# Kernel tuning notes

Measured on AMD Instinct MI355X. Metric: run time of the kernel, lower is better.

## Reference

```python
import jax, jax.numpy as jnp
import numpy as np

H, DK, DV = 16, 64, 64

def setup_inputs() -> dict:
    key = jax.random.key(0)
    ks = jax.random.split(key, 5)
    S, E = 2048, 1024
    return {
        "x": jax.random.normal(ks[0], (S, E), jnp.float32),
        "Wq": jax.random.normal(ks[1], (H * DK, E), jnp.float32) * 0.02,
        "Wk": jax.random.normal(ks[2], (H * DK, E), jnp.float32) * 0.02,
        "Wv": jax.random.normal(ks[3], (H * DV, E), jnp.float32) * 0.02,
        "Wo": jax.random.normal(ks[4], (H * DV, H * DV), jnp.float32) * 0.02,
    }

def reference(x, Wq, Wk, Wv, Wo):
    S = x.shape[0]
    # Fused QKV projections (equivalent to per-head Linear with concatenated weights)
    Q = (x @ Wq.T).reshape(S, H, DK).transpose(1, 0, 2)  # [H,S,dk]
    K = (x @ Wk.T).reshape(S, H, DK).transpose(1, 0, 2)  # [H,S,dk]
    V = (x @ Wv.T).reshape(S, H, DV).transpose(1, 0, 2)  # [H,S,dv]
    scale = 1.0 / np.sqrt(DK).astype(np.float32)
    scores = jnp.einsum('hsd,htd->hst', Q, K) * scale    # [H,S,S]
    weights = jax.nn.softmax(scores, axis=-1)
    A = jnp.einsum('hst,htv->hsv', weights, V)           # [H,S,dv]
    A1 = A.transpose(1, 0, 2).reshape(S, H * DV)         # concat heads on last dim
    return A1 @ Wo.T
```

## Files before the change

### kernel.cpp

```cpp
#include <hip/hip_runtime.h>
#include <hip/hip_bf16.h>
#include <stdint.h>

typedef uint16_t u16;
typedef uint32_t u32;
typedef float    f32x4  __attribute__((ext_vector_type(4)));
typedef __bf16   bf16x8 __attribute__((ext_vector_type(8)));
typedef uint16_t u16x8  __attribute__((ext_vector_type(8)));
typedef uint16_t u16x4  __attribute__((ext_vector_type(4)));
typedef uint32_t u32x4  __attribute__((ext_vector_type(4)));

#define HH 16
#define SS 2048
#define EE 1024
#define DD 64

__device__ inline u16 f2bf(float f) {
  uint32_t u = __builtin_bit_cast(uint32_t, f);
  u += 0x7fff + ((u >> 16) & 1);
  return (u16)(u >> 16);
}
__device__ inline float bf2f(u16 b) {
  return __builtin_bit_cast(float, (uint32_t)b << 16);
}

__device__ inline u32 cvtpk(float lo, float hi) {
  u32 r;
  asm("v_cvt_pk_bf16_f32 %0, %1, %2" : "=v"(r) : "v"(lo), "v"(hi));
  return r;
}

__device__ inline void gload_lds16(const void* g, void* l) {
  __builtin_amdgcn_global_load_lds(
      (const __attribute__((address_space(1))) uint32_t*)g,
      (__attribute__((address_space(3))) uint32_t*)l, 16, 0, 0);
}

__global__ __launch_bounds__(256) void convert_kernel(
    const float* __restrict__ x,  const float* __restrict__ wq,
    const float* __restrict__ wk, const float* __restrict__ wv,
    const float* __restrict__ wo,
    u16* __restrict__ xb, u16* __restrict__ wqkvb, u16* __restrict__ wob) {
  const int64_t M1 = 1024 * 1024;
  int64_t e = ((int64_t)blockIdx.x * 256 + threadIdx.x) * 4;
  const float* src; u16* dst; int64_t off;
  if (e < 2 * M1)      { src = x;  dst = xb;           off = e; }
  else if (e < 3 * M1) { src = wq; dst = wqkvb;        off = e - 2 * M1; }
  else if (e < 4 * M1) { src = wk; dst = wqkvb + M1;   off = e - 3 * M1; }
  else if (e < 5 * M1) { src = wv; dst = wqkvb + 2*M1; off = e - 4 * M1; }
  else                 { src = wo; dst = wob;          off = e - 5 * M1; }
  float4 v = *(const float4*)(src + off);
  u16x4 o;
  o[0] = f2bf(v.x); o[1] = f2bf(v.y); o[2] = f2bf(v.z); o[3] = f2bf(v.w);
  *(u16x4*)(dst + off) = o;
}

template <int EPI>
__global__ __launch_bounds__(256, 4) void gemm_kernel(
    const u16* __restrict__ A, const u16* __restrict__ B, int K, int N,
    u16* __restrict__ q_ws, u16* __restrict__ k_ws, u16* __restrict__ vt_ws,
    float* __restrict__ Cout) {
  constexpr int BM = 64, BN = 128, BK = 64;
  __shared__ __align__(16) u16 As[BM * BK];
  __shared__ __align__(16) u16 Bs[BN * BK];
  const int t = threadIdx.x;
  const int lane = t & 63, w = t >> 6;
  const int wr = w >> 1, wc = w & 1;
  const int fr = lane & 15, fg = lane >> 4;

  const int nwg = gridDim.x * gridDim.y;
  const int bid = blockIdx.y * gridDim.x + blockIdx.x;
  const int swz = (bid & 7) * (nwg >> 3) + (bid >> 3);
  const int m0 = (swz / gridDim.x) * BM, n0 = (swz % gridDim.x) * BN;

  f32x4 acc[2][4] = {};

  for (int k0 = 0; k0 < K; k0 += BK) {
#pragma unroll
    for (int it = 0; it < 2; ++it) {
      const int c = t + it * 256, row = c >> 3, sch = (c & 7) ^ (row & 7);
      gload_lds16(A + (int64_t)(m0 + row) * K + k0 + sch * 8,
                  As + (c & ~63) * 8);
    }
#pragma unroll
    for (int it = 0; it < 4; ++it) {
      const int c = t + it * 256, row = c >> 3, sch = (c & 7) ^ (row & 7);
      gload_lds16(B + (int64_t)(n0 + row) * K + k0 + sch * 8,
                  Bs + (c & ~63) * 8);
    }
    __syncthreads();
    bf16x8 af[2][2], bfr[4][2];
#pragma unroll
    for (int mi = 0; mi < 2; ++mi)
#pragma unroll
      for (int kc = 0; kc < 2; ++kc) {
        const int row = wr * 32 + mi * 16 + fr;
        const int cc = (kc * 4 + fg) ^ (row & 7);
        af[mi][kc] = __builtin_bit_cast(bf16x8, *(const u16x8*)&As[row * 64 + cc * 8]);
      }
#pragma unroll
    for (int ni = 0; ni < 4; ++ni)
#pragma unroll
      for (int kc = 0; kc < 2; ++kc) {
        const int row = wc * 64 + ni * 16 + fr;
        const int cc = (kc * 4 + fg) ^ (row & 7);
        bfr[ni][kc] = __builtin_bit_cast(bf16x8, *(const u16x8*)&Bs[row * 64 + cc * 8]);
      }
#pragma unroll
    for (int kc = 0; kc < 2; ++kc)
#pragma unroll
      for (int mi = 0; mi < 2; ++mi)
#pragma unroll
        for (int ni = 0; ni < 4; ++ni)
          acc[mi][ni] = __builtin_amdgcn_mfma_f32_16x16x32_bf16(
              af[mi][kc], bfr[ni][kc], acc[mi][ni], 0, 0, 0);
    __syncthreads();
  }

#pragma unroll
  for (int mi = 0; mi < 2; ++mi)
#pragma unroll
    for (int ni = 0; ni < 4; ++ni)
#pragma unroll
      for (int r = 0; r < 4; ++r) {
        const int m = m0 + wr * 32 + mi * 16 + fg * 4 + r;
        const int n = n0 + wc * 64 + ni * 16 + fr;
        const float v = acc[mi][ni][r];
        if constexpr (EPI == 0) {
          const int which = n >> 10, nn = n & 1023, h = nn >> 6, d = nn & 63;
          const u16 bv = f2bf(v);
          if (which == 0)      q_ws[((int64_t)h * SS + m) * DD + d] = bv;
          else if (which == 1) k_ws[((int64_t)h * SS + m) * DD + d] = bv;
          else                 vt_ws[((int64_t)h * DD + d) * SS + m] = bv;
        } else {
          Cout[(int64_t)m * N + n] = v;
        }
      }
}

__global__ __launch_bounds__(256, 4) void attn_kernel(
    const u16* __restrict__ q_ws, const u16* __restrict__ k_ws,
    const u16* __restrict__ vt_ws, u16* __restrict__ opart,
    float2* __restrict__ ml) {
  constexpr int NT2 = SS / 64 / 2;
  __shared__ __align__(16) u16 Ks[2][64 * 64];
  __shared__ __align__(16) u16 Vs[2][64 * 64];
  const int t = threadIdx.x;
  const int lane = t & 63, w = t >> 6;
  const int ql = lane & 15, g = lane >> 4;
  const int h = blockIdx.y, qb = blockIdx.x, sp = blockIdx.z;
  const int kt0 = sp * NT2;
  const int qbase = qb * 64 + w * 16;

  const u16* Qh = q_ws + ((int64_t)h * SS + qbase) * DD;
  const u16* Kh = k_ws + (int64_t)h * SS * DD;
  const u16* Vh = vt_ws + (int64_t)h * DD * SS;

  const int c0 = t, c1 = t + 256;
  const int r0 = c0 >> 3, ch0 = c0 & 7, r1 = c1 >> 3, ch1 = c1 & 7;
  const int d0 = r0 * 64 + ((ch0 ^ (r0 & 7)) * 8);
  const int d1 = r1 * 64 + ((ch1 ^ (r1 & 7)) * 8);

  bf16x8 qf[2];
#pragma unroll
  for (int dd = 0; dd < 2; ++dd)
    qf[dd] = __builtin_bit_cast(
        bf16x8, *(const u16x8*)(Qh + ql * DD + dd * 32 + g * 8));

  f32x4 o[4] = {};
  float m_run = -1e30f, l_run = 0.f;
  const float C2 = 0.18033688f;

  u16x8 gk0, gk1, gv0, gv1;
  gk0 = *(const u16x8*)(Kh + (int64_t)(kt0 * 64 + r0) * DD + ch0 * 8);
  gk1 = *(const u16x8*)(Kh + (int64_t)(kt0 * 64 + r1) * DD + ch1 * 8);
  gv0 = *(const u16x8*)(Vh + (int64_t)r0 * SS + kt0 * 64 + ch0 * 8);
  gv1 = *(const u16x8*)(Vh + (int64_t)r1 * SS + kt0 * 64 + ch1 * 8);
  *(u16x8*)&Ks[0][d0] = gk0; *(u16x8*)&Ks[0][d1] = gk1;
  *(u16x8*)&Vs[0][d0] = gv0; *(u16x8*)&Vs[0][d1] = gv1;
  __syncthreads();

  for (int kt = 0; kt < NT2; ++kt) {
    const int cur = kt & 1;
    if (kt + 1 < NT2) {
      const int kg = kt0 + kt + 1;
      const u16* Kn = Kh + (int64_t)kg * 64 * DD;
      const u16* Vn = Vh + kg * 64;
      gk0 = *(const u16x8*)(Kn + (int64_t)r0 * DD + ch0 * 8);
      gk1 = *(const u16x8*)(Kn + (int64_t)r1 * DD + ch1 * 8);
      gv0 = *(const u16x8*)(Vn + (int64_t)r0 * SS + ch0 * 8);
      gv1 = *(const u16x8*)(Vn + (int64_t)r1 * SS + ch1 * 8);
    }

    f32x4 s[4] = {};
    __builtin_amdgcn_s_setprio(1);
#pragma unroll
    for (int dd = 0; dd < 2; ++dd)
#pragma unroll
      for (int kb = 0; kb < 4; ++kb) {
        const int key = kb * 16 + ql;
        bf16x8 kf = __builtin_bit_cast(
            bf16x8,
            *(const u16x8*)&Ks[cur][key * 64 + (((dd * 4 + g) ^ (key & 7)) * 8)]);
        s[kb] = __builtin_amdgcn_mfma_f32_16x16x32_bf16(kf, qf[dd], s[kb], 0, 0, 0);
      }
    __builtin_amdgcn_s_setprio(0);

    float mx = s[0][0];
#pragma unroll
    for (int kb = 0; kb < 4; ++kb)
#pragma unroll
      for (int r = 0; r < 4; ++r) mx = fmaxf(mx, s[kb][r]);
    mx = fmaxf(mx, __shfl_xor(mx, 16));
    mx = fmaxf(mx, __shfl_xor(mx, 32));
    const float ts = mx * C2;
    const bool skip = __all(ts <= m_run + 8.0f);
    float sf = 1.f;
    if (!skip) {
      const float mnew = fmaxf(m_run, ts);
      sf = exp2f(m_run - mnew);
      m_run = mnew;
    }
    float p[4][4];
    float ls = 0.f;
#pragma unroll
    for (int kb = 0; kb < 4; ++kb)
#pragma unroll
      for (int r = 0; r < 4; ++r) {
        const float pv = exp2f(__fmaf_rn(s[kb][r], C2, -m_run));
        p[kb][r] = pv;
        ls += pv;
      }
    ls += __shfl_xor(ls, 16);
    ls += __shfl_xor(ls, 32);
    if (!skip) {
      l_run = __fmaf_rn(l_run, sf, ls);
#pragma unroll
      for (int r = 0; r < 4; ++r) {
        const float sfr = __shfl(sf, g * 4 + r);
#pragma unroll
        for (int nb = 0; nb < 4; ++nb) o[nb][r] *= sfr;
      }
    } else {
      l_run += ls;
    }

#pragma unroll
    for (int ks = 0; ks < 2; ++ks) {
      u32 x0 = cvtpk(p[2 * ks][0], p[2 * ks][1]);
      u32 x1 = cvtpk(p[2 * ks][2], p[2 * ks][3]);
      u32 y0 = cvtpk(p[2 * ks + 1][0], p[2 * ks + 1][1]);
      u32 y1 = cvtpk(p[2 * ks + 1][2], p[2 * ks + 1][3]);
      asm("v_permlane32_swap_b32 %0, %1" : "+v"(x0), "+v"(y0));
      asm("v_permlane16_swap_b32 %0, %1" : "+v"(x0), "+v"(y0));
      asm("v_permlane32_swap_b32 %0, %1" : "+v"(x1), "+v"(y1));
      asm("v_permlane16_swap_b32 %0, %1" : "+v"(x1), "+v"(y1));
      u32x4 aw; aw[0] = x0; aw[1] = x1; aw[2] = y0; aw[3] = y1;
      const bf16x8 pa = __builtin_bit_cast(bf16x8, aw);
      __builtin_amdgcn_s_setprio(1);
#pragma unroll
      for (int nb = 0; nb < 4; ++nb) {
        const int dv = nb * 16 + ql;
        bf16x8 vf = __builtin_bit_cast(
            bf16x8,
            *(const u16x8*)&Vs[cur][dv * 64 + (((ks * 4 + g) ^ (dv & 7)) * 8)]);
        o[nb] = __builtin_amdgcn_mfma_f32_16x16x32_bf16(pa, vf, o[nb], 0, 0, 0);
      }
      __builtin_amdgcn_s_setprio(0);
    }

    __syncthreads();
    if (kt + 1 < NT2) {
      u16* Kd = (u16*)&Ks[cur ^ 1][0];
      u16* Vd = (u16*)&Vs[cur ^ 1][0];
      *(u16x8*)&Kd[d0] = gk0; *(u16x8*)&Kd[d1] = gk1;
      *(u16x8*)&Vd[d0] = gv0; *(u16x8*)&Vd[d1] = gv1;
    }
    __syncthreads();
  }

  const int64_t rowbase = ((int64_t)sp * HH + h) * SS;
#pragma unroll
  for (int r = 0; r < 4; ++r) {
    const int q = qbase + g * 4 + r;
#pragma unroll
    for (int nb = 0; nb < 4; ++nb)
      opart[(rowbase + q) * DD + nb * 16 + ql] = f2bf(o[nb][r]);
  }
  if (g == 0) ml[rowbase + qbase + ql] = make_float2(m_run, l_run);
}

__global__ __launch_bounds__(256) void combine_kernel(
    const u16* __restrict__ opart, const float2* __restrict__ ml,
    u16* __restrict__ a_ws) {
  const int rid = blockIdx.x * 4 + (threadIdx.x >> 6);
  const int lane = threadIdx.x & 63;
  const int h = rid >> 11, q = rid & 2047;
  const float2 ml1 = ml[rid];
  const float2 ml2 = ml[HH * SS + rid];
  const float m = fmaxf(ml1.x, ml2.x);
  const float a1 = exp2f(ml1.x - m), a2 = exp2f(ml2.x - m);
  const float inv = 1.0f / __fmaf_rn(a1, ml1.y, a2 * ml2.y);
  const float o1 = bf2f(opart[(int64_t)rid * DD + lane]);
  const float o2 = bf2f(opart[((int64_t)HH * SS + rid) * DD + lane]);
  a_ws[(int64_t)q * (HH * DD) + h * DD + lane] =
      f2bf((a1 * o1 + a2 * o2) * inv);
}

extern "C" void kernel_launch(void* const* d_in, const int* in_sizes, int n_in,
                              void* d_out, int out_size, void* d_ws, size_t ws_size,
                              hipStream_t stream) {
  const float* x  = (const float*)d_in[0];
  const float* wq = (const float*)d_in[1];
  const float* wk = (const float*)d_in[2];
  const float* wv = (const float*)d_in[3];
  const float* wo = (const float*)d_in[4];
  char* ws = (char*)d_ws;
  const int64_t Mi = 1 << 20;
  u16* xb    = (u16*)(ws + 0 * Mi);
  u16* wqkv  = (u16*)(ws + 4 * Mi);
  u16* q_ws  = (u16*)(ws + 12 * Mi);
  u16* k_ws  = (u16*)(ws + 16 * Mi);
  u16* vt    = (u16*)(ws + 20 * Mi);
  u16* wob   = (u16*)(ws + 24 * Mi);
  u16*    opart = (u16*)(ws + 0 * Mi);
  float2* mlv   = (float2*)(ws + 8 * Mi);
  u16* a_ws  = (u16*)(ws + 12 * Mi);
  float* out = (float*)d_out;

  convert_kernel<<<6144, 256, 0, stream>>>(x, wq, wk, wv, wo, xb, wqkv, wob);

  gemm_kernel<0><<<dim3(3072 / 128, 2048 / 64), 256, 0, stream>>>(
      xb, wqkv, 1024, 3072, q_ws, k_ws, vt, nullptr);

  attn_kernel<<<dim3(SS / 64, HH, 2), 256, 0, stream>>>(q_ws, k_ws, vt, opart, mlv);

  combine_kernel<<<HH * SS / 4, 256, 0, stream>>>(opart, mlv, a_ws);

  gemm_kernel<1><<<dim3(1024 / 128, 2048 / 64), 256, 0, stream>>>(
      a_ws, wob, 1024, 1024, nullptr, nullptr, nullptr, out);
}
```

Baseline: 94.93 us.

## Software-pipeline attention with direct global-to-LDS loads and staggered QK/PV stages

Restructures the attention loop so that the QK^T MFMA for tile t runs alongside the softmax and PV for tile t-1. K and V tiles are loaded with direct global-to-LDS loads (gload_lds16) into a single double-buffered shared array, which removes the register-staged copy and one barrier per iteration. GEMM K and N also become template constants so the compiler can specialise them. The aim is to overlap memory latency and exp/shuffle work with matrix cores, at the cost of extra live registers (two score sets) and tighter ordering assumptions between async LDS writes and barriers.

```diff
diff --git a/kernel.cpp b/kernel.cpp
--- a/kernel.cpp
+++ b/kernel.cpp
@@ -55,9 +55,9 @@
   *(u16x4*)(dst + off) = o;
 }
 
-template <int EPI>
+template <int EPI, int K, int N>
 __global__ __launch_bounds__(256, 4) void gemm_kernel(
-    const u16* __restrict__ A, const u16* __restrict__ B, int K, int N,
+    const u16* __restrict__ A, const u16* __restrict__ B,
     u16* __restrict__ q_ws, u16* __restrict__ k_ws, u16* __restrict__ vt_ws,
     float* __restrict__ Cout) {
   constexpr int BM = 64, BN = 128, BK = 64;
@@ -143,8 +143,7 @@
     const u16* __restrict__ vt_ws, u16* __restrict__ opart,
     float2* __restrict__ ml) {
   constexpr int NT2 = SS / 64 / 2;
-  __shared__ __align__(16) u16 Ks[2][64 * 64];
-  __shared__ __align__(16) u16 Vs[2][64 * 64];
+  __shared__ __align__(16) u16 lds[16384];
   const int t = threadIdx.x;
   const int lane = t & 63, w = t >> 6;
   const int ql = lane & 15, g = lane >> 4;
@@ -153,13 +152,16 @@
   const int qbase = qb * 64 + w * 16;
 
   const u16* Qh = q_ws + ((int64_t)h * SS + qbase) * DD;
-  const u16* Kh = k_ws + (int64_t)h * SS * DD;
-  const u16* Vh = vt_ws + (int64_t)h * DD * SS;
-
-  const int c0 = t, c1 = t + 256;
-  const int r0 = c0 >> 3, ch0 = c0 & 7, r1 = c1 >> 3, ch1 = c1 & 7;
-  const int d0 = r0 * 64 + ((ch0 ^ (r0 & 7)) * 8);
-  const int d1 = r1 * 64 + ((ch1 ^ (r1 & 7)) * 8);
+  const u16* Kh = k_ws + ((int64_t)h * SS + kt0 * 64) * DD;
+  const u16* Vh = vt_ws + (int64_t)h * DD * SS + kt0 * 64;
+
+  const int r0 = t >> 3, ch = t & 7, r1 = (t + 256) >> 3;
+  const int sch0 = ch ^ (r0 & 7), sch1 = ch ^ (r1 & 7);
+  const int64_t ko0 = (int64_t)r0 * DD + sch0 * 8;
+  const int64_t ko1 = (int64_t)r1 * DD + sch1 * 8;
+  const int64_t vo0 = (int64_t)r0 * SS + sch0 * 8;
+  const int64_t vo1 = (int64_t)r1 * SS + sch1 * 8;
+  const int dst0 = (t & ~63) * 8, dst1 = (t & ~63) * 8 + 2048;
 
   bf16x8 qf[2];
 #pragma unroll
@@ -169,66 +171,50 @@
 
   f32x4 o[4] = {};
   float m_run = -1e30f, l_run = 0.f;
+  float sf = 1.f;
   const float C2 = 0.18033688f;
 
-  u16x8 gk0, gk1, gv0, gv1;
-  gk0 = *(const u16x8*)(Kh + (int64_t)(kt0 * 64 + r0) * DD + ch0 * 8);
-  gk1 = *(const u16x8*)(Kh + (int64_t)(kt0 * 64 + r1) * DD + ch1 * 8);
-  gv0 = *(const u16x8*)(Vh + (int64_t)r0 * SS + kt0 * 64 + ch0 * 8);
-  gv1 = *(const u16x8*)(Vh + (int64_t)r1 * SS + kt0 * 64 + ch1 * 8);
-  *(u16x8*)&Ks[0][d0] = gk0; *(u16x8*)&Ks[0][d1] = gk1;
-  *(u16x8*)&Vs[0][d0] = gv0; *(u16x8*)&Vs[0][d1] = gv1;
-  __syncthreads();
-
-  for (int kt = 0; kt < NT2; ++kt) {
-    const int cur = kt & 1;
-    if (kt + 1 < NT2) {
-      const int kg = kt0 + kt + 1;
-      const u16* Kn = Kh + (int64_t)kg * 64 * DD;
-      const u16* Vn = Vh + kg * 64;
-      gk0 = *(const u16x8*)(Kn + (int64_t)r0 * DD + ch0 * 8);
-      gk1 = *(const u16x8*)(Kn + (int64_t)r1 * DD + ch1 * 8);
-      gv0 = *(const u16x8*)(Vn + (int64_t)r0 * SS + ch0 * 8);
-      gv1 = *(const u16x8*)(Vn + (int64_t)r1 * SS + ch1 * 8);
-    }
-
-    f32x4 s[4] = {};
+  auto qk = [&](f32x4 (&s)[4], const int kb_) {
     __builtin_amdgcn_s_setprio(1);
 #pragma unroll
-    for (int dd = 0; dd < 2; ++dd)
-#pragma unroll
-      for (int kb = 0; kb < 4; ++kb) {
-        const int key = kb * 16 + ql;
+    for (int kb = 0; kb < 4; ++kb) {
+      const int key = kb * 16 + ql;
+      f32x4 z = {};
+#pragma unroll
+      for (int dd = 0; dd < 2; ++dd) {
         bf16x8 kf = __builtin_bit_cast(
             bf16x8,
-            *(const u16x8*)&Ks[cur][key * 64 + (((dd * 4 + g) ^ (key & 7)) * 8)]);
-        s[kb] = __builtin_amdgcn_mfma_f32_16x16x32_bf16(kf, qf[dd], s[kb], 0, 0, 0);
-      }
+            *(const u16x8*)&lds[kb_ * 4096 + key * 64 +
+                                (((dd * 4 + g) ^ (ql & 7)) * 8)]);
+        z = __builtin_amdgcn_mfma_f32_16x16x32_bf16(kf, qf[dd], z, 0, 0, 0);
+      }
+      s[kb] = z;
+    }
     __builtin_amdgcn_s_setprio(0);
-
-    float mx = s[0][0];
-#pragma unroll
-    for (int kb = 0; kb < 4; ++kb)
-#pragma unroll
-      for (int r = 0; r < 4; ++r) mx = fmaxf(mx, s[kb][r]);
+  };
+
+  auto smpv = [&](f32x4 (&s)[4], const int vb_) {
+    float m01 = fmaxf(fmaxf(s[0][0], s[0][1]), fmaxf(s[0][2], s[0][3]));
+    float m23 = fmaxf(fmaxf(s[1][0], s[1][1]), fmaxf(s[1][2], s[1][3]));
+    float m45 = fmaxf(fmaxf(s[2][0], s[2][1]), fmaxf(s[2][2], s[2][3]));
+    float m67 = fmaxf(fmaxf(s[3][0], s[3][1]), fmaxf(s[3][2], s[3][3]));
+    float mx = fmaxf(fmaxf(m01, m23), fmaxf(m45, m67));
     mx = fmaxf(mx, __shfl_xor(mx, 16));
     mx = fmaxf(mx, __shfl_xor(mx, 32));
     const float ts = mx * C2;
     const bool skip = __all(ts <= m_run + 8.0f);
-    float sf = 1.f;
     if (!skip) {
       const float mnew = fmaxf(m_run, ts);
       sf = exp2f(m_run - mnew);
       m_run = mnew;
     }
-    float p[4][4];
     float ls = 0.f;
 #pragma unroll
     for (int kb = 0; kb < 4; ++kb)
 #pragma unroll
       for (int r = 0; r < 4; ++r) {
         const float pv = exp2f(__fmaf_rn(s[kb][r], C2, -m_run));
-        p[kb][r] = pv;
+        s[kb][r] = pv;
         ls += pv;
       }
     ls += __shfl_xor(ls, 16);
@@ -244,13 +230,12 @@
     } else {
       l_run += ls;
     }
-
 #pragma unroll
     for (int ks = 0; ks < 2; ++ks) {
-      u32 x0 = cvtpk(p[2 * ks][0], p[2 * ks][1]);
-      u32 x1 = cvtpk(p[2 * ks][2], p[2 * ks][3]);
-      u32 y0 = cvtpk(p[2 * ks + 1][0], p[2 * ks + 1][1]);
-      u32 y1 = cvtpk(p[2 * ks + 1][2], p[2 * ks + 1][3]);
+      u32 x0 = cvtpk(s[2 * ks][0], s[2 * ks][1]);
+      u32 x1 = cvtpk(s[2 * ks][2], s[2 * ks][3]);
+      u32 y0 = cvtpk(s[2 * ks + 1][0], s[2 * ks + 1][1]);
+      u32 y1 = cvtpk(s[2 * ks + 1][2], s[2 * ks + 1][3]);
       asm("v_permlane32_swap_b32 %0, %1" : "+v"(x0), "+v"(y0));
       asm("v_permlane16_swap_b32 %0, %1" : "+v"(x0), "+v"(y0));
       asm("v_permlane32_swap_b32 %0, %1" : "+v"(x1), "+v"(y1));
@@ -263,21 +248,43 @@
         const int dv = nb * 16 + ql;
         bf16x8 vf = __builtin_bit_cast(
             bf16x8,
-            *(const u16x8*)&Vs[cur][dv * 64 + (((ks * 4 + g) ^ (dv & 7)) * 8)]);
+            *(const u16x8*)&lds[8192 + vb_ * 4096 + dv * 64 +
+                                (((ks * 4 + g) ^ (ql & 7)) * 8)]);
         o[nb] = __builtin_amdgcn_mfma_f32_16x16x32_bf16(pa, vf, o[nb], 0, 0, 0);
       }
       __builtin_amdgcn_s_setprio(0);
     }
-
+  };
+
+  gload_lds16(Kh + ko0, lds + dst0);
+  gload_lds16(Kh + ko1, lds + dst1);
+
+  f32x4 sA[4], sB[4];
+#pragma unroll
+  for (int tt = 0; tt < NT2; ++tt) {
     __syncthreads();
-    if (kt + 1 < NT2) {
-      u16* Kd = (u16*)&Ks[cur ^ 1][0];
-      u16* Vd = (u16*)&Vs[cur ^ 1][0];
-      *(u16x8*)&Kd[d0] = gk0; *(u16x8*)&Kd[d1] = gk1;
-      *(u16x8*)&Vd[d0] = gv0; *(u16x8*)&Vd[d1] = gv1;
-    }
-    __syncthreads();
+    if (tt + 1 < NT2) {
+      const u16* Kn = Kh + (int64_t)(tt + 1) * 64 * DD;
+      const int kb = ((tt + 1) & 1) * 4096;
+      gload_lds16(Kn + ko0, lds + kb + dst0);
+      gload_lds16(Kn + ko1, lds + kb + dst1);
+    }
+    {
+      const u16* Vn = Vh + tt * 64;
+      const int vb = 8192 + (tt & 1) * 4096;
+      gload_lds16(Vn + vo0, lds + vb + dst0);
+      gload_lds16(Vn + vo1, lds + vb + dst1);
+    }
+    if (tt & 1) {
+      qk(sB, tt & 1);
+      smpv(sA, (tt - 1) & 1);
+    } else {
+      qk(sA, tt & 1);
+      if (tt > 0) smpv(sB, (tt - 1) & 1);
+    }
   }
+  __syncthreads();
+  smpv(sB, (NT2 - 1) & 1);
 
   const int64_t rowbase = ((int64_t)sp * HH + h) * SS;
 #pragma unroll
@@ -330,13 +337,13 @@
 
   convert_kernel<<<6144, 256, 0, stream>>>(x, wq, wk, wv, wo, xb, wqkv, wob);
 
-  gemm_kernel<0><<<dim3(3072 / 128, 2048 / 64), 256, 0, stream>>>(
-      xb, wqkv, 1024, 3072, q_ws, k_ws, vt, nullptr);
+  gemm_kernel<0, 1024, 3072><<<dim3(3072 / 128, 2048 / 64), 256, 0, stream>>>(
+      xb, wqkv, q_ws, k_ws, vt, nullptr);
 
   attn_kernel<<<dim3(SS / 64, HH, 2), 256, 0, stream>>>(q_ws, k_ws, vt, opart, mlv);
 
   combine_kernel<<<HH * SS / 4, 256, 0, stream>>>(opart, mlv, a_ws);
 
-  gemm_kernel<1><<<dim3(1024 / 128, 2048 / 64), 256, 0, stream>>>(
-      a_ws, wob, 1024, 1024, nullptr, nullptr, nullptr, out);
-}
+  gemm_kernel<1, 1024, 1024><<<dim3(1024 / 128, 2048 / 64), 256, 0, stream>>>(
+      a_ws, wob, nullptr, nullptr, nullptr, out);
+}
```

After: 92.74 us. 1.02x faster.
